# Kernel optimization log

Hardware: AMD Instinct MI355X
Metric: run time of the kernel (lower is better)

The kernel has to match this reference:

```python
import jax, jax.numpy as jnp
import numpy as np

# SH constants (standard 3DGS eval_sh, degree 3)
C0 = 0.28209479177387814
C1 = 0.4886025119029199
C2 = (1.0925484305920792, -1.0925484305920792, 0.31539156525252005, -1.0925484305920792, 0.5462742152960396)
C3 = (-0.5900435899266435, 2.890611442640554, -0.4570457994644658, 0.3731763325901154, -0.4570457994644658, 1.445305721320277, -0.5900435899266435)

N_GAUSS = 4096
N_PTS = 32768
CHUNK = 4096  # math-identical to torch's 16384 chunking (pure concat of independent points)


def quat_to_rot(q):
    # q: (N,4) normalized, (w,x,y,z) as in 3DGS build_rotation
    r, x, y, z = q[:, 0], q[:, 1], q[:, 2], q[:, 3]
    R = jnp.stack([
        jnp.stack([1 - 2 * (y * y + z * z), 2 * (x * y - r * z), 2 * (x * z + r * y)], -1),
        jnp.stack([2 * (x * y + r * z), 1 - 2 * (x * x + z * z), 2 * (y * z - r * x)], -1),
        jnp.stack([2 * (x * z - r * y), 2 * (y * z + r * x), 1 - 2 * (x * x + y * y)], -1),
    ], axis=-2)  # (N,3,3)
    return R


def eval_sh3(sh, dirs):
    # sh: (N,16) scalar SH coeffs; dirs: (C,N,3) unit directions -> (C,N)
    x, y, z = dirs[..., 0], dirs[..., 1], dirs[..., 2]
    xx, yy, zz = x * x, y * y, z * z
    xy, yz, xz = x * y, y * z, x * z
    s = sh[None]  # (1,N,16)
    res = C0 * s[..., 0]
    res = res - C1 * y * s[..., 1] + C1 * z * s[..., 2] - C1 * x * s[..., 3]
    res = (res + C2[0] * xy * s[..., 4] + C2[1] * yz * s[..., 5]
           + C2[2] * (2 * zz - xx - yy) * s[..., 6]
           + C2[3] * xz * s[..., 7] + C2[4] * (xx - yy) * s[..., 8])
    res = (res + C3[0] * y * (3 * xx - yy) * s[..., 9] + C3[1] * xy * z * s[..., 10]
           + C3[2] * y * (4 * zz - xx - yy) * s[..., 11]
           + C3[3] * z * (2 * zz - 3 * xx - 3 * yy) * s[..., 12]
           + C3[4] * x * (4 * zz - xx - yy) * s[..., 13]
           + C3[5] * z * (xx - yy) * s[..., 14]
           + C3[6] * x * (xx - yy - 3 * zz) * s[..., 15])
    return res


def setup_inputs() -> dict:
    key = jax.random.key(0)
    ks = jax.random.split(key, 9)
    return {
        "network_pts": jax.random.normal(ks[0], (N_PTS, 3), jnp.float32),
        "network_view": jax.random.normal(ks[1], (N_PTS, 3), jnp.float32),
        "network_tx": jax.random.normal(ks[2], (N_PTS, 3), jnp.float32),
        "xyz": jax.random.normal(ks[3], (N_GAUSS, 3), jnp.float32),
        "sh_dc": jax.random.normal(ks[4], (N_GAUSS, 1), jnp.float32),
        "sh_rest": 0.1 * jax.random.normal(ks[5], (N_GAUSS, 15), jnp.float32),
        "scaling": jnp.float32(-3.0) + 0.2 * jax.random.normal(ks[6], (N_GAUSS, 3), jnp.float32),
        "rotation": jax.random.normal(ks[7], (N_GAUSS, 4), jnp.float32),
        "opacity_logit": jax.random.normal(ks[8], (N_GAUSS, 1), jnp.float32),
    }


def reference(network_pts, network_view, network_tx, xyz, sh_dc, sh_rest, scaling, rotation, opacity_logit):
    # activations, matching GaussianModel.setup_functions
    sh = jnp.concatenate([sh_dc, sh_rest], axis=1)            # (N,16)
    s = jnp.exp(scaling)                                      # (N,3)
    q = rotation / jnp.linalg.norm(rotation, axis=1, keepdims=True)
    R = quat_to_rot(q)                                        # (N,3,3)
    # precision = (L L^T)^{-1} with L = R diag(s)  =>  R diag(1/s^2) R^T
    prec = jnp.einsum('nij,nj,nkj->nik', R, 1.0 / (s * s), R)  # (N,3,3)
    op = jax.nn.sigmoid(opacity_logit)[:, 0]                  # (N,)

    pts = network_pts.reshape(-1, CHUNK, 3)

    def chunk_fn(p):  # p: (C,3)
        diff = p[:, None, :] - xyz[None, :, :]                # (C,N,3)
        maha = jnp.einsum('cni,nij,cnj->cn', diff, prec, diff)
        w = op[None, :] * jnp.exp(-0.5 * maha)                # (C,N)
        # dir_pp = xyz - query_point, normalized (as in get_magnitude)
        dirs = -diff / jnp.linalg.norm(diff, axis=-1, keepdims=True)
        mag = jnp.maximum(eval_sh3(sh, dirs), 0.0)            # (C,N)
        return w.sum(axis=1), (w * mag).sum(axis=1)

    opac_c, sig_c = jax.lax.map(chunk_fn, pts)
    return opac_c.reshape(-1), sig_c.reshape(-1)
```

## Files before the change

### kernel.cpp

```cpp
#include <hip/hip_runtime.h>
#include <hip/hip_bf16.h>

#define N_GAUSS 4096
#define N_PTS   32768
#define BLOCK   256
#define NCHUNK  32
#define NBLK_PT 128
#define GSTRIDE 32
#define NCELL   4096
#define NBIN    32
#define RECCAP  128

#define SH_C0  0.28209479177387814f
#define SH_C1  0.4886025119029199f

#define WS_GP     0
#define WS_GHIST  131072
#define WS_CELLID 135168
#define WS_SPTS   167936
#define WS_ACC    299008
#define WS_HPART  364544
#define WS_ACT    495616
#define WS_NACT   1019904

__device__ __forceinline__ int cell_of(float x, float y, float z) {
    int cx = min(15, max(0, (int)((x + 3.2f) * 2.5f)));
    int cy = min(15, max(0, (int)((y + 3.2f) * 2.5f)));
    int cz = min(15, max(0, (int)((z + 3.2f) * 2.5f)));
    int ex = (cx & 1) | ((cx & 2) << 2) | ((cx & 4) << 4) | ((cx & 8) << 6);
    int ey = (cy & 1) | ((cy & 2) << 2) | ((cy & 4) << 4) | ((cy & 8) << 6);
    int ez = (cz & 1) | ((cz & 2) << 2) | ((cz & 4) << 4) | ((cz & 8) << 6);
    return ex | (ey << 1) | (ez << 2);
}

__global__ __launch_bounds__(1024) void binprep_kernel(
    const float* __restrict__ pts, const float* __restrict__ xyz,
    const float* __restrict__ sh_dc, const float* __restrict__ sh_rest,
    const float* __restrict__ scaling, const float* __restrict__ rotation,
    const float* __restrict__ opl, float* __restrict__ gp,
    int* __restrict__ cellid, int* __restrict__ hpart, float* __restrict__ acc)
{
    const int t = threadIdx.x, bx = blockIdx.x;

    if (bx >= 36) {
        float4* a4 = (float4*)acc;
        int base = (bx - 36) * 2048 + t;
        a4[base]        = make_float4(0.f, 0.f, 0.f, 0.f);
        a4[base + 1024] = make_float4(0.f, 0.f, 0.f, 0.f);
        return;
    }
    if (bx >= 32) {
        int g = (bx - 32) * 1024 + t;
        float s0 = scaling[3*g+0], s1 = scaling[3*g+1], s2 = scaling[3*g+2];
        float i0 = __expf(-2.0f * s0);
        float i1 = __expf(-2.0f * s1);
        float i2 = __expf(-2.0f * s2);
        float maxs2 = __expf(2.0f * fmaxf(s0, fmaxf(s1, s2)));

        float r = rotation[4*g+0], x = rotation[4*g+1];
        float y = rotation[4*g+2], z = rotation[4*g+3];
        float n = rsqrtf(r*r + x*x + y*y + z*z);
        r *= n; x *= n; y *= n; z *= n;
        float R00 = 1.f - 2.f*(y*y + z*z), R01 = 2.f*(x*y - r*z), R02 = 2.f*(x*z + r*y);
        float R10 = 2.f*(x*y + r*z), R11 = 1.f - 2.f*(x*x + z*z), R12 = 2.f*(y*z - r*x);
        float R20 = 2.f*(x*z - r*y), R21 = 2.f*(y*z + r*x), R22 = 1.f - 2.f*(x*x + y*y);

        float pxx = 0.5f*(R00*R00*i0 + R01*R01*i1 + R02*R02*i2);
        float pxy = 0.5f*(R00*R10*i0 + R01*R11*i1 + R02*R12*i2);
        float pxz = 0.5f*(R00*R20*i0 + R01*R21*i1 + R02*R22*i2);
        float pyy = 0.5f*(R10*R10*i0 + R11*R11*i1 + R12*R12*i2);
        float pyz = 0.5f*(R10*R20*i0 + R11*R21*i1 + R12*R22*i2);
        float pzz = 0.5f*(R20*R20*i0 + R21*R21*i1 + R22*R22*i2);

        float op   = 1.f / (1.f + __expf(-opl[g]));
        float lnop = __logf(op);
        float Tg   = 2.0f * maxs2 * (lnop + 16.0f);

        const float* sr = sh_rest + (size_t)g * 15;
        float4* G4 = (float4*)(gp + (size_t)g * GSTRIDE);
        G4[0] = make_float4(xyz[3*g+0], xyz[3*g+1], xyz[3*g+2], Tg);
        G4[1] = make_float4(pxx, pxy, pxz, pyy);
        G4[2] = make_float4(pyz, pzz, lnop, 0.f);
        G4[3] = make_float4( SH_C0 * sh_dc[g],
                            -SH_C1 * sr[0],
                             SH_C1 * sr[1],
                            -SH_C1 * sr[2]);
        G4[4] = make_float4( 1.0925484305920792f  * sr[3],
                            -1.0925484305920792f  * sr[4],
                             0.31539156525252005f * sr[5],
                            -1.0925484305920792f  * sr[6]);
        G4[5] = make_float4( 0.5462742152960396f  * sr[7],
                            -0.5900435899266435f  * sr[8],
                             2.890611442640554f   * sr[9],
                            -0.4570457994644658f  * sr[10]);
        G4[6] = make_float4( 0.3731763325901154f  * sr[11],
                            -0.4570457994644658f  * sr[12],
                             1.445305721320277f   * sr[13],
                            -0.5900435899266435f  * sr[14]);
        G4[7] = make_float4(0.f, 0.f, 0.f, 0.f);
        return;
    }

    __shared__ int s_hist[NCELL];
    #pragma unroll
    for (int i = 0; i < 4; ++i) s_hist[t + i * 1024] = 0;
    __syncthreads();
    {
        int p = bx * 1024 + t;
        float x = pts[3*p+0], y = pts[3*p+1], z = pts[3*p+2];
        int cell = cell_of(x, y, z);
        cellid[p] = cell;
        atomicAdd(&s_hist[cell], 1);
    }
    __syncthreads();
    #pragma unroll
    for (int i = 0; i < 4; ++i) {
        int c = t + i * 1024;
        hpart[bx * NCELL + c] = s_hist[c];
    }
}

__global__ __launch_bounds__(1024) void scan_kernel(
    const int* __restrict__ hpart, int* __restrict__ ghist)
{
    __shared__ int s_wsum[16];
    const int t = threadIdx.x;
    const int lane = t & 63, wv = t >> 6;
    const int b = t * 4;

    int4 c = make_int4(0, 0, 0, 0);
    #pragma unroll
    for (int k = 0; k < NBIN; ++k) {
        int4 h = *(const int4*)(hpart + k * NCELL + b);
        c.x += h.x; c.y += h.y; c.z += h.z; c.w += h.w;
    }
    int s = c.x + c.y + c.z + c.w;

    int incl = s;
    #pragma unroll
    for (int off = 1; off < 64; off <<= 1) {
        int v = __shfl_up(incl, off);
        if (lane >= off) incl += v;
    }
    if (lane == 63) s_wsum[wv] = incl;
    __syncthreads();
    if (wv == 0) {
        int ws = (lane < 16) ? s_wsum[lane] : 0;
        int wincl = ws;
        #pragma unroll
        for (int off = 1; off < 16; off <<= 1) {
            int v = __shfl_up(wincl, off);
            if (lane >= off) wincl += v;
        }
        if (lane < 16) s_wsum[lane] = wincl - ws;
    }
    __syncthreads();

    int excl = s_wsum[wv] + (incl - s);
    ghist[b]   = excl;
    ghist[b+1] = excl + c.x;
    ghist[b+2] = excl + c.x + c.y;
    ghist[b+3] = excl + c.x + c.y + c.z;
}

__global__ __launch_bounds__(256) void scatter_kernel(
    const float* __restrict__ pts, const int* __restrict__ cellid,
    int* __restrict__ ghist, float4* __restrict__ spts)
{
    int p = blockIdx.x * 256 + threadIdx.x;
    float x = pts[3*p+0], y = pts[3*p+1], z = pts[3*p+2];
    int pos = atomicAdd(&ghist[cellid[p]], 1);
    spts[pos] = make_float4(x, y, z, __int_as_float(p));
}

__global__ __launch_bounds__(BLOCK) void cull_kernel(
    const float4* __restrict__ spts, const float4* __restrict__ gp4,
    int* __restrict__ actlist, int* __restrict__ nactg)
{
    __shared__ float s_min[4][3], s_max[4][3];
    __shared__ int s_n;
    __shared__ int s_list[N_GAUSS];

    const int tid = threadIdx.x;
    const int pb  = blockIdx.x;
    float4 P = spts[pb * 256 + tid];
    const float px = P.x, py = P.y, pz = P.z;

    float mnx = px, mxx = px, mny = py, mxy = py, mnz = pz, mxz = pz;
    #pragma unroll
    for (int off = 32; off >= 1; off >>= 1) {
        mnx = fminf(mnx, __shfl_xor(mnx, off));
        mxx = fmaxf(mxx, __shfl_xor(mxx, off));
        mny = fminf(mny, __shfl_xor(mny, off));
        mxy = fmaxf(mxy, __shfl_xor(mxy, off));
        mnz = fminf(mnz, __shfl_xor(mnz, off));
        mxz = fmaxf(mxz, __shfl_xor(mxz, off));
    }
    const int wave = tid >> 6;
    if ((tid & 63) == 0) {
        s_min[wave][0] = mnx; s_min[wave][1] = mny; s_min[wave][2] = mnz;
        s_max[wave][0] = mxx; s_max[wave][1] = mxy; s_max[wave][2] = mxz;
    }
    if (tid == 0) s_n = 0;
    __syncthreads();
    const float bmnx = fminf(fminf(s_min[0][0], s_min[1][0]), fminf(s_min[2][0], s_min[3][0]));
    const float bmny = fminf(fminf(s_min[0][1], s_min[1][1]), fminf(s_min[2][1], s_min[3][1]));
    const float bmnz = fminf(fminf(s_min[0][2], s_min[1][2]), fminf(s_min[2][2], s_min[3][2]));
    const float bmxx = fmaxf(fmaxf(s_max[0][0], s_max[1][0]), fmaxf(s_max[2][0], s_max[3][0]));
    const float bmxy = fmaxf(fmaxf(s_max[0][1], s_max[1][1]), fmaxf(s_max[2][1], s_max[3][1]));
    const float bmxz = fmaxf(fmaxf(s_max[0][2], s_max[1][2]), fmaxf(s_max[2][2], s_max[3][2]));

    for (int r = 0; r < N_GAUSS / BLOCK; ++r) {
        const int gg = r * BLOCK + tid;
        float4 c = gp4[(size_t)gg << 3];
        float ddx = fmaxf(0.f, fmaxf(bmnx - c.x, c.x - bmxx));
        float ddy = fmaxf(0.f, fmaxf(bmny - c.y, c.y - bmxy));
        float ddz = fmaxf(0.f, fmaxf(bmnz - c.z, c.z - bmxz));
        float dd2 = ddx*ddx + ddy*ddy + ddz*ddz;
        if (dd2 <= c.w) {
            int slot = atomicAdd(&s_n, 1);
            s_list[slot] = gg;
        }
    }
    __syncthreads();
    const int n = s_n;
    for (int i = tid; i < n; i += BLOCK) actlist[pb * N_GAUSS + i] = s_list[i];
    if (tid == 0) nactg[pb] = n;
}

__device__ __forceinline__ void eval_one(
    const float4* R, float dx, float dy, float dz, float d2,
    float& opac, float& sig)
{
    float4 q1 = R[1], q2 = R[2];
    float vx = q1.x*dx + q1.y*dy + q1.z*dz;
    float vy = q1.y*dx + q1.w*dy + q2.x*dz;
    float vz = q1.z*dx + q2.x*dy + q2.y*dz;
    float maha = dx*vx + dy*vy + dz*vz;
    float w = __expf(q2.z - maha);
    opac += w;

    if (__any(w > 1e-9f)) {
        float4 q3 = R[3], q4 = R[4], q5 = R[5], q6 = R[6];
        float rinv = rsqrtf(d2);
        float x = -dx * rinv, y = -dy * rinv, z = -dz * rinv;
        float xx = x*x, yy = y*y, zz = z*z;
        float xy = x*y, yz = y*z, xz = x*z;

        float res = q3.x;
        res += y * q3.y;
        res += z * q3.z;
        res += x * q3.w;
        res += xy * q4.x;
        res += yz * q4.y;
        res += (3.f*zz - 1.f) * q4.z;
        res += xz * q4.w;
        float xxmyy = xx - yy;
        res += xxmyy * q5.x;
        res += y * (3.f*xx - yy) * q5.y;
        res += (xy * z) * q5.z;
        float f5z1 = 5.f*zz - 1.f;
        res += y * f5z1 * q5.w;
        res += z * (5.f*zz - 3.f) * q6.x;
        res += x * f5z1 * q6.y;
        res += z * xxmyy * q6.z;
        res += x * (xxmyy - 3.f*zz) * q6.w;

        sig += w * fmaxf(res, 0.f);
    }
}

__global__ __launch_bounds__(BLOCK) void eval_kernel(
    const float4* __restrict__ spts, const float4* __restrict__ gp4,
    const int* __restrict__ actlist, const int* __restrict__ nactg,
    float* __restrict__ acc)
{
    __shared__ int s_idx[RECCAP];
    __shared__ float4 s_rec[RECCAP * 8];

    const int tid = threadIdx.x;
    const int ck  = blockIdx.x;
    const int pb  = blockIdx.y;

    const int nact = nactg[pb];
    const int c0 = (nact * ck) / NCHUNK;
    const int c1 = (nact * (ck + 1)) / NCHUNK;
    const int cnt = c1 - c0;
    if (cnt == 0) return;

    float4 P = spts[pb * 256 + tid];
    if (tid < cnt) s_idx[tid] = actlist[pb * N_GAUSS + c0 + tid];
    __syncthreads();

    for (int idx = tid; idx < cnt * 8; idx += BLOCK) {
        int rec = idx >> 3, q = idx & 7;
        s_rec[idx] = gp4[((size_t)s_idx[rec] << 3) + q];
    }
    __syncthreads();

    const float px = P.x, py = P.y, pz = P.z;
    float opac = 0.f, sig = 0.f;
    for (int j = 0; j < cnt; j += 2) {
        const bool has1 = (j + 1 < cnt);
        const float4* A = &s_rec[j * 8];
        const float4* B = &s_rec[(has1 ? j + 1 : j) * 8];

        float4 aq0 = A[0];
        float4 bq0 = B[0];
        float adx = px - aq0.x, ady = py - aq0.y, adz = pz - aq0.z;
        float bdx = px - bq0.x, bdy = py - bq0.y, bdz = pz - bq0.z;
        float ad2 = adx*adx + ady*ady + adz*adz;
        float bd2 = bdx*bdx + bdy*bdy + bdz*bdz;

        if (!__all(ad2 > aq0.w)) eval_one(A, adx, ady, adz, ad2, opac, sig);
        if (has1 && !__all(bd2 > bq0.w)) eval_one(B, bdx, bdy, bdz, bd2, opac, sig);
    }

    const int pos = pb * 256 + tid;
    atomicAdd(&acc[pos], opac);
    atomicAdd(&acc[N_PTS + pos], sig);
}

__global__ __launch_bounds__(256) void permute_kernel(
    const float* __restrict__ acc, const float4* __restrict__ spts,
    float* __restrict__ out)
{
    int p = blockIdx.x * 256 + threadIdx.x;
    int orig = __float_as_int(spts[p].w);
    out[orig] = acc[p];
    out[N_PTS + orig] = acc[N_PTS + p];
}

extern "C" void kernel_launch(void* const* d_in, const int* in_sizes, int n_in,
                              void* d_out, int out_size, void* d_ws, size_t ws_size,
                              hipStream_t stream) {
    const float* pts      = (const float*)d_in[0];
    const float* xyz      = (const float*)d_in[3];
    const float* sh_dc    = (const float*)d_in[4];
    const float* sh_rest  = (const float*)d_in[5];
    const float* scaling  = (const float*)d_in[6];
    const float* rotation = (const float*)d_in[7];
    const float* opl      = (const float*)d_in[8];

    float*  out     = (float*)d_out;
    float*  wsf     = (float*)d_ws;
    float*  gp      = wsf + WS_GP;
    int*    ghist   = (int*)(wsf + WS_GHIST);
    int*    cellid  = (int*)(wsf + WS_CELLID);
    float4* spts    = (float4*)(wsf + WS_SPTS);
    float*  acc     = wsf + WS_ACC;
    int*    hpart   = (int*)(wsf + WS_HPART);
    int*    actlist = (int*)(wsf + WS_ACT);
    int*    nactg   = (int*)(wsf + WS_NACT);

    binprep_kernel<<<dim3(44), dim3(1024), 0, stream>>>(
        pts, xyz, sh_dc, sh_rest, scaling, rotation, opl, gp, cellid, hpart, acc);
    scan_kernel<<<dim3(1), dim3(1024), 0, stream>>>(hpart, ghist);
    scatter_kernel<<<dim3(NBLK_PT), dim3(256), 0, stream>>>(pts, cellid, ghist, spts);

    cull_kernel<<<dim3(NBLK_PT), dim3(BLOCK), 0, stream>>>(
        spts, (const float4*)gp, actlist, nactg);
    eval_kernel<<<dim3(NCHUNK, NBLK_PT), dim3(BLOCK), 0, stream>>>(
        spts, (const float4*)gp, actlist, nactg, acc);
    permute_kernel<<<dim3(NBLK_PT), dim3(256), 0, stream>>>(acc, spts, out);
}
```

Baseline: 123.2 us.

## Fuse cull into eval kernel with ballot-based compaction and halve histogram blocks

Removes the separate cull kernel and its global active-list round trip. Each eval block now recomputes the point block's bounding box, tests all Gaussians against it, and compacts the survivors into shared memory through wave ballots and a prefix scan. This drops one launch and the actlist/nactg traffic, and makes the active-list order deterministic. The cost is that the cull work and the strided reads of Gaussian headers are repeated for every chunk block of the same point block, which is 32 times as many. The binning prep also uses 16 histogram blocks of 2048 points each instead of 32 blocks of 1024.

```diff
diff --git a/kernel.cpp b/kernel.cpp
--- a/kernel.cpp
+++ b/kernel.cpp
@@ -8,7 +8,7 @@
 #define NBLK_PT 128
 #define GSTRIDE 32
 #define NCELL   4096
-#define NBIN    32
+#define NBIN    16
 #define RECCAP  128
 
 #define SH_C0  0.28209479177387814f
@@ -20,8 +20,6 @@
 #define WS_SPTS   167936
 #define WS_ACC    299008
 #define WS_HPART  364544
-#define WS_ACT    495616
-#define WS_NACT   1019904
 
 __device__ __forceinline__ int cell_of(float x, float y, float z) {
     int cx = min(15, max(0, (int)((x + 3.2f) * 2.5f)));
@@ -42,15 +40,15 @@
 {
     const int t = threadIdx.x, bx = blockIdx.x;
 
-    if (bx >= 36) {
+    if (bx >= 20) {
         float4* a4 = (float4*)acc;
-        int base = (bx - 36) * 2048 + t;
+        int base = (bx - 20) * 2048 + t;
         a4[base]        = make_float4(0.f, 0.f, 0.f, 0.f);
         a4[base + 1024] = make_float4(0.f, 0.f, 0.f, 0.f);
         return;
     }
-    if (bx >= 32) {
-        int g = (bx - 32) * 1024 + t;
+    if (bx >= 16) {
+        int g = (bx - 16) * 1024 + t;
         float s0 = scaling[3*g+0], s1 = scaling[3*g+1], s2 = scaling[3*g+2];
         float i0 = __expf(-2.0f * s0);
         float i1 = __expf(-2.0f * s1);
@@ -105,8 +103,9 @@
     #pragma unroll
     for (int i = 0; i < 4; ++i) s_hist[t + i * 1024] = 0;
     __syncthreads();
-    {
-        int p = bx * 1024 + t;
+    #pragma unroll
+    for (int k = 0; k < 2; ++k) {
+        int p = bx * 2048 + k * 1024 + t;
         float x = pts[3*p+0], y = pts[3*p+1], z = pts[3*p+2];
         int cell = cell_of(x, y, z);
         cellid[p] = cell;
@@ -171,61 +170,6 @@
     float x = pts[3*p+0], y = pts[3*p+1], z = pts[3*p+2];
     int pos = atomicAdd(&ghist[cellid[p]], 1);
     spts[pos] = make_float4(x, y, z, __int_as_float(p));
-}
-
-__global__ __launch_bounds__(BLOCK) void cull_kernel(
-    const float4* __restrict__ spts, const float4* __restrict__ gp4,
-    int* __restrict__ actlist, int* __restrict__ nactg)
-{
-    __shared__ float s_min[4][3], s_max[4][3];
-    __shared__ int s_n;
-    __shared__ int s_list[N_GAUSS];
-
-    const int tid = threadIdx.x;
-    const int pb  = blockIdx.x;
-    float4 P = spts[pb * 256 + tid];
-    const float px = P.x, py = P.y, pz = P.z;
-
-    float mnx = px, mxx = px, mny = py, mxy = py, mnz = pz, mxz = pz;
-    #pragma unroll
-    for (int off = 32; off >= 1; off >>= 1) {
-        mnx = fminf(mnx, __shfl_xor(mnx, off));
-        mxx = fmaxf(mxx, __shfl_xor(mxx, off));
-        mny = fminf(mny, __shfl_xor(mny, off));
-        mxy = fmaxf(mxy, __shfl_xor(mxy, off));
-        mnz = fminf(mnz, __shfl_xor(mnz, off));
-        mxz = fmaxf(mxz, __shfl_xor(mxz, off));
-    }
-    const int wave = tid >> 6;
-    if ((tid & 63) == 0) {
-        s_min[wave][0] = mnx; s_min[wave][1] = mny; s_min[wave][2] = mnz;
-        s_max[wave][0] = mxx; s_max[wave][1] = mxy; s_max[wave][2] = mxz;
-    }
-    if (tid == 0) s_n = 0;
-    __syncthreads();
-    const float bmnx = fminf(fminf(s_min[0][0], s_min[1][0]), fminf(s_min[2][0], s_min[3][0]));
-    const float bmny = fminf(fminf(s_min[0][1], s_min[1][1]), fminf(s_min[2][1], s_min[3][1]));
-    const float bmnz = fminf(fminf(s_min[0][2], s_min[1][2]), fminf(s_min[2][2], s_min[3][2]));
-    const float bmxx = fmaxf(fmaxf(s_max[0][0], s_max[1][0]), fmaxf(s_max[2][0], s_max[3][0]));
-    const float bmxy = fmaxf(fmaxf(s_max[0][1], s_max[1][1]), fmaxf(s_max[2][1], s_max[3][1]));
-    const float bmxz = fmaxf(fmaxf(s_max[0][2], s_max[1][2]), fmaxf(s_max[2][2], s_max[3][2]));
-
-    for (int r = 0; r < N_GAUSS / BLOCK; ++r) {
-        const int gg = r * BLOCK + tid;
-        float4 c = gp4[(size_t)gg << 3];
-        float ddx = fmaxf(0.f, fmaxf(bmnx - c.x, c.x - bmxx));
-        float ddy = fmaxf(0.f, fmaxf(bmny - c.y, c.y - bmxy));
-        float ddz = fmaxf(0.f, fmaxf(bmnz - c.z, c.z - bmxz));
-        float dd2 = ddx*ddx + ddy*ddy + ddz*ddz;
-        if (dd2 <= c.w) {
-            int slot = atomicAdd(&s_n, 1);
-            s_list[slot] = gg;
-        }
-    }
-    __syncthreads();
-    const int n = s_n;
-    for (int i = tid; i < n; i += BLOCK) actlist[pb * N_GAUSS + i] = s_list[i];
-    if (tid == 0) nactg[pb] = n;
 }
 
 __device__ __forceinline__ void eval_one(
@@ -270,35 +214,97 @@
     }
 }
 
-__global__ __launch_bounds__(BLOCK) void eval_kernel(
+__global__ __launch_bounds__(BLOCK) void culleval_kernel(
     const float4* __restrict__ spts, const float4* __restrict__ gp4,
-    const int* __restrict__ actlist, const int* __restrict__ nactg,
     float* __restrict__ acc)
 {
-    __shared__ int s_idx[RECCAP];
+    __shared__ float s_min[4][3], s_max[4][3];
+    __shared__ unsigned long long s_mask[64];
+    __shared__ int s_base[64];
+    __shared__ int s_n;
+    __shared__ unsigned short s_list[N_GAUSS];
     __shared__ float4 s_rec[RECCAP * 8];
 
-    const int tid = threadIdx.x;
-    const int ck  = blockIdx.x;
-    const int pb  = blockIdx.y;
-
-    const int nact = nactg[pb];
+    const int tid  = threadIdx.x;
+    const int ck   = blockIdx.x;
+    const int pb   = blockIdx.y;
+    const int lane = tid & 63;
+    const int wv   = tid >> 6;
+
+    float4 P = spts[pb * 256 + tid];
+    const float px = P.x, py = P.y, pz = P.z;
+
+    float mnx = px, mxx = px, mny = py, mxy = py, mnz = pz, mxz = pz;
+    #pragma unroll
+    for (int off = 32; off >= 1; off >>= 1) {
+        mnx = fminf(mnx, __shfl_xor(mnx, off));
+        mxx = fmaxf(mxx, __shfl_xor(mxx, off));
+        mny = fminf(mny, __shfl_xor(mny, off));
+        mxy = fmaxf(mxy, __shfl_xor(mxy, off));
+        mnz = fminf(mnz, __shfl_xor(mnz, off));
+        mxz = fmaxf(mxz, __shfl_xor(mxz, off));
+    }
+    if (lane == 0) {
+        s_min[wv][0] = mnx; s_min[wv][1] = mny; s_min[wv][2] = mnz;
+        s_max[wv][0] = mxx; s_max[wv][1] = mxy; s_max[wv][2] = mxz;
+    }
+    __syncthreads();
+    const float bmnx = fminf(fminf(s_min[0][0], s_min[1][0]), fminf(s_min[2][0], s_min[3][0]));
+    const float bmny = fminf(fminf(s_min[0][1], s_min[1][1]), fminf(s_min[2][1], s_min[3][1]));
+    const float bmnz = fminf(fminf(s_min[0][2], s_min[1][2]), fminf(s_min[2][2], s_min[3][2]));
+    const float bmxx = fmaxf(fmaxf(s_max[0][0], s_max[1][0]), fmaxf(s_max[2][0], s_max[3][0]));
+    const float bmxy = fmaxf(fmaxf(s_max[0][1], s_max[1][1]), fmaxf(s_max[2][1], s_max[3][1]));
+    const float bmxz = fmaxf(fmaxf(s_max[0][2], s_max[1][2]), fmaxf(s_max[2][2], s_max[3][2]));
+
+    #pragma unroll
+    for (int r = 0; r < N_GAUSS / BLOCK; ++r) {
+        const int gg = r * BLOCK + tid;
+        float4 c = gp4[(size_t)gg << 3];
+        float ddx = fmaxf(0.f, fmaxf(bmnx - c.x, c.x - bmxx));
+        float ddy = fmaxf(0.f, fmaxf(bmny - c.y, c.y - bmxy));
+        float ddz = fmaxf(0.f, fmaxf(bmnz - c.z, c.z - bmxz));
+        float dd2 = ddx*ddx + ddy*ddy + ddz*ddz;
+        unsigned long long m = __ballot(dd2 <= c.w);
+        if (lane == 0) s_mask[r * 4 + wv] = m;
+    }
+    __syncthreads();
+
+    if (tid < 64) {
+        int cme = (int)__popcll(s_mask[tid]);
+        int incl = cme;
+        #pragma unroll
+        for (int off = 1; off < 64; off <<= 1) {
+            int v = __shfl_up(incl, off);
+            if (tid >= off) incl += v;
+        }
+        s_base[tid] = incl - cme;
+        if (tid == 63) s_n = incl;
+    }
+    __syncthreads();
+    const int nact = s_n;
+
+    #pragma unroll
+    for (int r = 0; r < N_GAUSS / BLOCK; ++r) {
+        unsigned long long m = s_mask[r * 4 + wv];
+        if ((m >> lane) & 1ull) {
+            int pos = s_base[r * 4 + wv] +
+                      (int)__popcll(m & ((1ull << lane) - 1ull));
+            s_list[pos] = (unsigned short)(r * BLOCK + tid);
+        }
+    }
+    __syncthreads();
+
     const int c0 = (nact * ck) / NCHUNK;
     const int c1 = (nact * (ck + 1)) / NCHUNK;
     const int cnt = c1 - c0;
     if (cnt == 0) return;
 
-    float4 P = spts[pb * 256 + tid];
-    if (tid < cnt) s_idx[tid] = actlist[pb * N_GAUSS + c0 + tid];
-    __syncthreads();
-
     for (int idx = tid; idx < cnt * 8; idx += BLOCK) {
         int rec = idx >> 3, q = idx & 7;
-        s_rec[idx] = gp4[((size_t)s_idx[rec] << 3) + q];
-    }
-    __syncthreads();
-
-    const float px = P.x, py = P.y, pz = P.z;
+        s_rec[idx] = gp4[((size_t)s_list[c0 + rec] << 3) + q];
+    }
+    __syncthreads();
+
     float opac = 0.f, sig = 0.f;
     for (int j = 0; j < cnt; j += 2) {
         const bool has1 = (j + 1 < cnt);
@@ -342,25 +348,21 @@
     const float* rotation = (const float*)d_in[7];
     const float* opl      = (const float*)d_in[8];
 
-    float*  out     = (float*)d_out;
-    float*  wsf     = (float*)d_ws;
-    float*  gp      = wsf + WS_GP;
-    int*    ghist   = (int*)(wsf + WS_GHIST);
-    int*    cellid  = (int*)(wsf + WS_CELLID);
-    float4* spts    = (float4*)(wsf + WS_SPTS);
-    float*  acc     = wsf + WS_ACC;
-    int*    hpart   = (int*)(wsf + WS_HPART);
-    int*    actlist = (int*)(wsf + WS_ACT);
-    int*    nactg   = (int*)(wsf + WS_NACT);
-
-    binprep_kernel<<<dim3(44), dim3(1024), 0, stream>>>(
+    float*  out    = (float*)d_out;
+    float*  wsf    = (float*)d_ws;
+    float*  gp     = wsf + WS_GP;
+    int*    ghist  = (int*)(wsf + WS_GHIST);
+    int*    cellid = (int*)(wsf + WS_CELLID);
+    float4* spts   = (float4*)(wsf + WS_SPTS);
+    float*  acc    = wsf + WS_ACC;
+    int*    hpart  = (int*)(wsf + WS_HPART);
+
+    binprep_kernel<<<dim3(28), dim3(1024), 0, stream>>>(
         pts, xyz, sh_dc, sh_rest, scaling, rotation, opl, gp, cellid, hpart, acc);
     scan_kernel<<<dim3(1), dim3(1024), 0, stream>>>(hpart, ghist);
     scatter_kernel<<<dim3(NBLK_PT), dim3(256), 0, stream>>>(pts, cellid, ghist, spts);
 
-    cull_kernel<<<dim3(NBLK_PT), dim3(BLOCK), 0, stream>>>(
-        spts, (const float4*)gp, actlist, nactg);
-    eval_kernel<<<dim3(NCHUNK, NBLK_PT), dim3(BLOCK), 0, stream>>>(
-        spts, (const float4*)gp, actlist, nactg, acc);
+    culleval_kernel<<<dim3(NCHUNK, NBLK_PT), dim3(BLOCK), 0, stream>>>(
+        spts, (const float4*)gp, acc);
     permute_kernel<<<dim3(NBLK_PT), dim3(256), 0, stream>>>(acc, spts, out);
 }
```

After: 170.6 us. +38.5%, slower.
